# Kernel optimization log

Measured on AMD Instinct MI355X. Metric: run time of the kernel, lower is better.

Reference implementation:

```python
import jax, jax.numpy as jnp
import numpy as np

GRID_SIZE = 5
SPLINE_ORDER = 3
NUM_COEFF = GRID_SIZE + SPLINE_ORDER  # 8
L = 3
B, I, H = 4096, 256, 512
EPS = 1e-5


def make_grid(in_features):
    # efficient-kan default grid over [-1, 1] extended by spline_order knots each side
    h = 2.0 / GRID_SIZE
    g = jnp.arange(-SPLINE_ORDER, GRID_SIZE + SPLINE_ORDER + 1, dtype=jnp.float32) * h - 1.0
    return jnp.broadcast_to(g, (in_features, g.shape[0]))  # (in, G+2k+1)


def b_splines(x, grid):
    # x: (B, in), grid: (in, G+2k+1) -> (B, in, G+k) via Cox-de-Boor recursion
    xg = x[..., None]
    bases = ((xg >= grid[:, :-1]) & (xg < grid[:, 1:])).astype(x.dtype)
    for j in range(1, SPLINE_ORDER + 1):
        left = (xg - grid[:, :-(j + 1)]) / (grid[:, j:-1] - grid[:, :-(j + 1)])
        right = (grid[:, j + 1:] - xg) / (grid[:, j + 1:] - grid[:, 1:-j])
        bases = left * bases[..., :-1] + right * bases[..., 1:]
    return bases


def kan_linear(x, base_w, spline_w, grid):
    # base path: SiLU(x) @ W_base^T ; spline path: sum over (in, coeff)
    base = jax.nn.silu(x) @ base_w.T
    spl = jnp.einsum('bik,oik->bo', b_splines(x, grid), spline_w)
    return base + spl


def layer_norm(x, g, b):
    mu = jnp.mean(x, axis=-1, keepdims=True)
    var = jnp.var(x, axis=-1, keepdims=True)
    return (x - mu) / jnp.sqrt(var + EPS) * g + b


def _sublayer(z_prev, wx_b, wx_s, wh_b, wh_s, hz_b, hz_s, phi_b, phi_s,
              hh_w, hh_b, ln_g, ln_b, x_t, grid_in, grid_h):
    s_t = kan_linear(x_t, wx_b, wx_s, grid_in) + kan_linear(z_prev, wh_b, wh_s, grid_h)
    o_t = kan_linear(s_t, phi_b, phi_s, grid_h)
    z_t = layer_norm(z_prev @ hh_w.T + hh_b + kan_linear(o_t, hz_b, hz_s, grid_h), ln_g, ln_b)
    return o_t, z_t


def setup_inputs() -> dict:
    key = jax.random.key(0)
    ks = jax.random.split(key, 24)
    s = 0.05  # small init to keep gates/splines in sane range
    inp = {
        'x_t': jax.random.normal(ks[0], (B, I), jnp.float32),
        'h_prev': jax.random.normal(ks[1], (B, H), jnp.float32),
        'c_prev': jax.random.normal(ks[2], (B, H), jnp.float32),
        'z_prev': jax.random.normal(ks[3], (L, B, H), jnp.float32),
        'wx_base': jax.random.normal(ks[4], (L, H, I), jnp.float32) * s,
        'wx_spline': jax.random.normal(ks[5], (L, H, I, NUM_COEFF), jnp.float32) * s,
        'wh_base': jax.random.normal(ks[6], (L, H, H), jnp.float32) * s,
        'wh_spline': jax.random.normal(ks[7], (L, H, H, NUM_COEFF), jnp.float32) * s,
        'hz_base': jax.random.normal(ks[8], (L, H, H), jnp.float32) * s,
        'hz_spline': jax.random.normal(ks[9], (L, H, H, NUM_COEFF), jnp.float32) * s,
        'phi_base': jax.random.normal(ks[10], (L, H, H), jnp.float32) * s,
        'phi_spline': jax.random.normal(ks[11], (L, H, H, NUM_COEFF), jnp.float32) * s,
        'hh_w': jax.random.normal(ks[12], (L, H, H), jnp.float32) * s,
        'hh_b': jax.random.normal(ks[13], (L, H), jnp.float32) * s,
        'ln_g': jnp.ones((L, H), jnp.float32),
        'ln_b': jnp.zeros((L, H), jnp.float32),
        'f_w': jax.random.normal(ks[14], (H, I + H), jnp.float32) * s,
        'f_b': jax.random.normal(ks[15], (H,), jnp.float32) * s,
        'i_w': jax.random.normal(ks[16], (H, I + H), jnp.float32) * s,
        'i_b': jax.random.normal(ks[17], (H,), jnp.float32) * s,
        'g_w': jax.random.normal(ks[18], (H, I + H), jnp.float32) * s,
        'g_b': jax.random.normal(ks[19], (H,), jnp.float32) * s,
        'o_w': jax.random.normal(ks[20], (H, L * H), jnp.float32) * s,
        'o_b': jax.random.normal(ks[21], (H,), jnp.float32) * s,
    }
    return inp


def reference(x_t, h_prev, c_prev, z_prev, wx_base, wx_spline, wh_base, wh_spline,
              hz_base, hz_spline, phi_base, phi_spline, hh_w, hh_b, ln_g, ln_b,
              f_w, f_b, i_w, i_b, g_w, g_b, o_w, o_b):
    grid_in = make_grid(I)
    grid_h = make_grid(H)
    cat = jnp.concatenate([x_t, h_prev], axis=-1)  # (B, I+H)
    f_t = jax.nn.sigmoid(cat @ f_w.T + f_b)
    i_t = jax.nn.sigmoid(cat @ i_w.T + i_b)
    g_t = jnp.tanh(cat @ g_w.T + g_b)
    # vmap the RKAN sublayer over the L stacked sublayers
    sub = jax.vmap(_sublayer, in_axes=(0,) * 13 + (None, None, None))
    o_all, z_all = sub(z_prev, wx_base, wx_spline, wh_base, wh_spline,
                       hz_base, hz_spline, phi_base, phi_spline,
                       hh_w, hh_b, ln_g, ln_b, x_t, grid_in, grid_h)
    # concat sublayer phi outputs: (L,B,H) -> (B, L*H)
    r_t = jnp.transpose(o_all, (1, 0, 2)).reshape(B, L * H)
    o_t = jax.nn.sigmoid(r_t @ o_w.T + o_b)
    c_t = f_t * c_prev + i_t * g_t
    h_t = o_t * jnp.tanh(c_t)
    return h_t, c_t, z_all
```

## Files before the change

kernel.cpp:

```cpp
#include <hip/hip_runtime.h>

typedef __attribute__((ext_vector_type(8))) short short8;
typedef __attribute__((ext_vector_type(4))) float floatx4;

__device__ inline short f2bf(float v) {
    unsigned u = __builtin_bit_cast(unsigned, v);
    unsigned r = (u + 0x7fffu + ((u >> 16) & 1u)) >> 16;
    return (short)r;
}
__device__ inline float bf2f(short s) {
    unsigned u = ((unsigned)(unsigned short)s) << 16;
    return __builtin_bit_cast(float, u);
}

__device__ inline void spline8(float v, short* arr) {
    float u = (v + 2.2f) * 2.5f;
    float fj = floorf(u);
    int jj = (int)fj;
    float t1 = u - fj;
    float ok = (jj >= 0 && jj <= 10) ? (1.f / 6.f) : 0.f;
    float t2 = t1 * t1, t3 = t2 * t1;
    float omt = 1.f - t1;
    short sw0 = f2bf(omt * omt * omt * ok);
    short sw1 = f2bf((3.f * t3 - 6.f * t2 + 4.f) * ok);
    short sw2 = f2bf((-3.f * t3 + 3.f * t2 + 3.f * t1 + 1.f) * ok);
    short sw3 = f2bf(t3 * ok);
#pragma unroll
    for (int s = 0; s < 8; ++s) {
        int rr = s - jj + 3;
        arr[s] = (rr == 0) ? sw0 : (rr == 1) ? sw1 : (rr == 2) ? sw2
                 : (rr == 3) ? sw3 : (short)0;
    }
}

__global__ __launch_bounds__(256, 3) void gemm128(
    int S, int Kh,
    const short* __restrict__ A0, int lda0, long sA0, int K0,
    const short* __restrict__ W0, int ldw0, long sW0,
    const short* __restrict__ A1, int lda1, long sA1, int K1,
    const short* __restrict__ W1, int ldw1, long sW1,
    float* __restrict__ C, int ldc, long sC, long sSplit)
{
    __shared__ short As[128 * 32];
    __shared__ short Ws[128 * 32];
    const int t = threadIdx.x;
    int n = blockIdx.x + (blockIdx.y << 5) + (blockIdx.z << 7);
    int k8 = n & 7, j = n >> 3;
    int byi = j & 3;
    int t2 = j >> 2;
    int bxi = k8 * 4 + (t2 & 3);
    int bzi = t2 >> 2;
    const int z = bzi / S, s = bzi % S;
    const int bm = bxi * 128, bn = byi * 128;
    const int lane = t & 63, w = t >> 6;
    const int wm = (w >> 1) * 64, wn = (w & 1) * 64;
    const int lrow = lane & 15, quad = lane >> 4;

    floatx4 acc[4][4] = {};

    const int kbeg = s * Kh, kend = kbeg + Kh;

    const short* A = A0 + (long)z * sA0;
    const short* W = W0 + (long)z * sW0;
    int lda = lda0, ldw = ldw0;
    int kb = kbeg, ke = (kend < K0) ? kend : K0;

    for (int seg = 0; seg < 2; ++seg) {
        for (int kv = kb; kv < ke; kv += 32) {
#pragma unroll
            for (int cj = 0; cj < 2; ++cj) {
                int c = cj * 256 + t;
                int row = c >> 2, cg = (c & 3) * 8;
                const short* gp = A + (long)(bm + row) * lda + kv + cg;
                __builtin_amdgcn_global_load_lds(
                    (const __attribute__((address_space(1))) void*)gp,
                    (__attribute__((address_space(3))) void*)(As + c * 8), 16, 0, 0);
                const short* gq = W + (long)(bn + row) * ldw + kv + cg;
                __builtin_amdgcn_global_load_lds(
                    (const __attribute__((address_space(1))) void*)gq,
                    (__attribute__((address_space(3))) void*)(Ws + c * 8), 16, 0, 0);
            }
            __syncthreads();
            short8 af[4], bfr[4];
#pragma unroll
            for (int mi = 0; mi < 4; ++mi)
                af[mi] = *(const short8*)(As + (wm + mi * 16 + lrow) * 32 + quad * 8);
#pragma unroll
            for (int ni = 0; ni < 4; ++ni)
                bfr[ni] = *(const short8*)(Ws + (wn + ni * 16 + lrow) * 32 + quad * 8);
#pragma unroll
            for (int mi = 0; mi < 4; ++mi)
#pragma unroll
                for (int ni = 0; ni < 4; ++ni)
                    acc[mi][ni] = __builtin_amdgcn_mfma_f32_16x16x32_bf16(
                        af[mi], bfr[ni], acc[mi][ni], 0, 0, 0);
            __syncthreads();
        }
        A = A1 + (long)z * sA1;
        W = W1 + (long)z * sW1;
        lda = lda1; ldw = ldw1;
        kb = ((kbeg > K0) ? kbeg : K0) - K0;
        ke = kend - K0;
    }

    float* Cz = C + (long)z * sC + (long)s * sSplit;
#pragma unroll
    for (int mi = 0; mi < 4; ++mi)
#pragma unroll
        for (int ni = 0; ni < 4; ++ni)
#pragma unroll
            for (int r = 0; r < 4; ++r) {
                int row = bm + wm + mi * 16 + quad * 4 + r;
                int col = bn + wn + ni * 16 + lrow;
                Cz[(long)row * ldc + col] = acc[mi][ni][r];
            }
}

__global__ __launch_bounds__(256) void gemm64(
    int swz,
    const short* __restrict__ A0, int lda0, long sA0, int K0,
    const short* __restrict__ W0, int ldw0, long sW0,
    const short* __restrict__ A1, int lda1, long sA1, int K1,
    const short* __restrict__ W1, int ldw1, long sW1,
    short* __restrict__ C, int ldc, long sC)
{
    __shared__ short As[64 * 32];
    __shared__ short Ws[128 * 32];
    const int t = threadIdx.x;
    int bxi = blockIdx.x, byi = blockIdx.y, bzi = blockIdx.z;
    if (swz) {
        int n = bxi + (byi << 6) + (bzi << 8);
        int k = n & 7, j = n >> 3;
        byi = j & 3;
        bxi = k * 8 + ((j >> 2) & 7);
        bzi = j >> 5;
    }
    const int z = bzi;
    const int bm = bxi * 64;
    const int bn = byi * 128;
    const int lane = t & 63, w = t >> 6;
    const int wm = (w >> 1) * 32, wn = (w & 1) * 64;
    const int lrow = lane & 15, quad = lane >> 4;

    floatx4 acc[2][4] = {};

    const short* A = A0 + (long)z * sA0;
    const short* W = W0 + (long)z * sW0;
    int K = K0, lda = lda0, ldw = ldw0;

    for (int seg = 0; seg < 2; ++seg) {
        for (int k0 = 0; k0 < K; k0 += 32) {
            {
                int row = t >> 2, cg = (t & 3) * 8;
                const short* gp = A + (long)(bm + row) * lda + k0 + cg;
                __builtin_amdgcn_global_load_lds(
                    (const __attribute__((address_space(1))) void*)gp,
                    (__attribute__((address_space(3))) void*)(As + t * 8), 16, 0, 0);
            }
#pragma unroll
            for (int j = 0; j < 2; ++j) {
                int cj = j * 256 + t;
                int row = cj >> 2, cg = (cj & 3) * 8;
                const short* gq = W + (long)(bn + row) * ldw + k0 + cg;
                __builtin_amdgcn_global_load_lds(
                    (const __attribute__((address_space(1))) void*)gq,
                    (__attribute__((address_space(3))) void*)(Ws + cj * 8), 16, 0, 0);
            }
            __syncthreads();
            short8 af[2], bfr[4];
#pragma unroll
            for (int mi = 0; mi < 2; ++mi)
                af[mi] = *(const short8*)(As + (wm + mi * 16 + lrow) * 32 + quad * 8);
#pragma unroll
            for (int ni = 0; ni < 4; ++ni)
                bfr[ni] = *(const short8*)(Ws + (wn + ni * 16 + lrow) * 32 + quad * 8);
#pragma unroll
            for (int mi = 0; mi < 2; ++mi)
#pragma unroll
                for (int ni = 0; ni < 4; ++ni)
                    acc[mi][ni] = __builtin_amdgcn_mfma_f32_16x16x32_bf16(
                        af[mi], bfr[ni], acc[mi][ni], 0, 0, 0);
            __syncthreads();
        }
        A = A1 + (long)z * sA1; W = W1 + (long)z * sW1;
        K = K1; lda = lda1; ldw = ldw1;
    }

    short* Cz = C + (long)z * sC;
#pragma unroll
    for (int mi = 0; mi < 2; ++mi)
#pragma unroll
        for (int ni = 0; ni < 4; ++ni)
#pragma unroll
            for (int r = 0; r < 4; ++r) {
                int row = bm + wm + mi * 16 + quad * 4 + r;
                int col = bn + wn + ni * 16 + lrow;
                Cz[(long)row * ldc + col] = f2bf(acc[mi][ni][r]);
            }
}

__global__ __launch_bounds__(256) void megapack(
    const float* __restrict__ wx_b, const float* __restrict__ wx_s,
    const float* __restrict__ wh_b, const float* __restrict__ wh_s,
    const float* __restrict__ hz_b, const float* __restrict__ hz_s,
    const float* __restrict__ phi_b, const float* __restrict__ phi_s,
    const float* __restrict__ hh_w, const float* __restrict__ o_w,
    const float* __restrict__ f_w, const float* __restrict__ i_w,
    const float* __restrict__ g_w,
    short* __restrict__ Wx, short* __restrict__ Wh, short* __restrict__ Whz,
    short* __restrict__ Wphi, short* __restrict__ HHb, short* __restrict__ OWb,
    short* __restrict__ Wg)
{
    int bid = blockIdx.x, tid = threadIdx.x;
    if (bid < 13824) {
        long idx = (long)bid * 256 + tid;
        int r = (int)(idx / 2304), c = (int)(idx % 2304);
        float v = (c < 256) ? wx_b[(long)r * 256 + c]
                            : wx_s[(long)r * 2048 + (c - 256)];
        Wx[idx] = f2bf(v);
    } else if (bid < 96768) {
        int jb = bid - 13824;
        int job = jb / 27648, lb = jb % 27648;
        const float* bp = (job == 0) ? wh_b : (job == 1) ? hz_b : phi_b;
        const float* sp = (job == 0) ? wh_s : (job == 1) ? hz_s : phi_s;
        short* dp = (job == 0) ? Wh : (job == 1) ? Whz : Wphi;
        long idx = (long)lb * 256 + tid;
        int r = (int)(idx / 4608), c = (int)(idx % 4608);
        float v = (c < 512) ? bp[(long)r * 512 + c]
                            : sp[(long)r * 4096 + (c - 512)];
        dp[idx] = f2bf(v);
    } else if (bid < 99840) {
        long idx = (long)(bid - 96768) * 256 + tid;
        HHb[idx] = f2bf(hh_w[idx]);
    } else if (bid < 102912) {
        long idx = (long)(bid - 99840) * 256 + tid;
        OWb[idx] = f2bf(o_w[idx]);
    } else if (bid < 104448) {
        long idx = (long)(bid - 102912) * 256 + tid;
        Wg[idx] = f2bf(f_w[idx]);
    } else if (bid < 105984) {
        long idx = (long)(bid - 104448) * 256 + tid;
        Wg[393216 + idx] = f2bf(i_w[idx]);
    } else {
        long idx = (long)(bid - 105984) * 256 + tid;
        Wg[786432 + idx] = f2bf(g_w[idx]);
    }
}

__global__ __launch_bounds__(256) void prep_acts(
    const float* __restrict__ x_t, const float* __restrict__ h_prev,
    const float* __restrict__ z_prev,
    short* __restrict__ Xe, short* __restrict__ Agate,
    short* __restrict__ Ze, short* __restrict__ zraw)
{
    int bid = blockIdx.x, tid = threadIdx.x;
    if (bid < 4096) {
        int r = bid, i = tid;
        float v = x_t[(long)r * 256 + i];
        Agate[(long)r * 768 + i] = f2bf(v);
        long ob = (long)r * 2304;
        Xe[ob + i] = f2bf(v / (1.f + __expf(-v)));
        short arr[8];
        spline8(v, arr);
        *(short8*)(Xe + ob + 256 + (long)i * 8) = *(const short8*)arr;
    } else if (bid < 12288) {
        long idx = (long)(bid - 4096) * 256 + tid;
        long b = idx >> 9; int hh = (int)(idx & 511);
        Agate[b * 768 + 256 + hh] = f2bf(h_prev[idx]);
    } else {
        int j = bid - 12288;
        int r = j >> 1, i = (j & 1) * 256 + tid;
        float v = z_prev[(long)r * 512 + i];
        zraw[(long)r * 512 + i] = f2bf(v);
        long ob = (long)r * 4608;
        Ze[ob + i] = f2bf(v / (1.f + __expf(-v)));
        short arr[8];
        spline8(v, arr);
        *(short8*)(Ze + ob + 512 + (long)i * 8) = *(const short8*)arr;
    }
}

__global__ __launch_bounds__(256) void expand_pair(
    const float* __restrict__ P, long split_off, int inF,
    short* __restrict__ out, short* __restrict__ compact)
{
    int i = blockIdx.x * 256 + threadIdx.x;
    int r = blockIdx.y;
    long idx = (long)r * inF + i;
    float v = P[idx] + P[idx + split_off];
    if (compact) compact[idx] = f2bf(v);

    long ob = (long)r * inF * 9;
    out[ob + i] = f2bf(v / (1.f + __expf(-v)));

    short arr[8];
    spline8(v, arr);
    *(short8*)(out + ob + inF + (long)i * 8) = *(const short8*)arr;
}

__global__ __launch_bounds__(256) void ln_pair(const float* __restrict__ P,
                                               long split_off,
                                               const float* __restrict__ hh_b,
                                               const float* __restrict__ ln_g,
                                               const float* __restrict__ ln_b,
                                               float* __restrict__ out)
{
    int row = blockIdx.x;
    int l = row >> 12;
    int t = threadIdx.x;
    long base = (long)row * 512;
    float v0 = P[base + t]       + P[base + t + split_off]       + hh_b[l * 512 + t];
    float v1 = P[base + t + 256] + P[base + t + 256 + split_off] + hh_b[l * 512 + t + 256];
    float s = v0 + v1, sq = v0 * v0 + v1 * v1;
#pragma unroll
    for (int off = 32; off; off >>= 1) {
        s += __shfl_down(s, off);
        sq += __shfl_down(sq, off);
    }
    __shared__ float ls[4], lq[4];
    int w = t >> 6, lane = t & 63;
    if (lane == 0) { ls[w] = s; lq[w] = sq; }
    __syncthreads();
    float S = ls[0] + ls[1] + ls[2] + ls[3];
    float Q = lq[0] + lq[1] + lq[2] + lq[3];
    float mu = S * (1.f / 512.f);
    float var = Q * (1.f / 512.f) - mu * mu;
    float rstd = rsqrtf(var + 1e-5f);
    float* o = out + (long)row * 512;
    o[t]       = (v0 - mu) * rstd * ln_g[l * 512 + t]       + ln_b[l * 512 + t];
    o[t + 256] = (v1 - mu) * rstd * ln_g[l * 512 + t + 256] + ln_b[l * 512 + t + 256];
}

__global__ __launch_bounds__(256) void cell_epilogue(const short* __restrict__ gates,
                                                     const short* __restrict__ opre,
                                                     const float* __restrict__ c_prev,
                                                     const float* __restrict__ f_b,
                                                     const float* __restrict__ i_b,
                                                     const float* __restrict__ g_b,
                                                     const float* __restrict__ o_b,
                                                     float* __restrict__ out)
{
    long idx = blockIdx.x * 256L + threadIdx.x;
    long b = idx >> 9; int h = (int)(idx & 511);
    const short* g = gates + b * 1536;
    float fp = bf2f(g[h]) + f_b[h];
    float ip = bf2f(g[512 + h]) + i_b[h];
    float gp = bf2f(g[1024 + h]) + g_b[h];
    float op = bf2f(opre[idx]) + o_b[h];
    float ft = 1.f / (1.f + __expf(-fp));
    float it = 1.f / (1.f + __expf(-ip));
    float gt = tanhf(gp);
    float ot = 1.f / (1.f + __expf(-op));
    float c = ft * c_prev[idx] + it * gt;
    out[idx] = ot * tanhf(c);
    out[idx + 2097152] = c;
}

extern "C" void kernel_launch(void* const* d_in, const int* in_sizes, int n_in,
                              void* d_out, int out_size, void* d_ws, size_t ws_size,
                              hipStream_t stream)
{
    const float* x_t       = (const float*)d_in[0];
    const float* h_prev    = (const float*)d_in[1];
    const float* c_prev    = (const float*)d_in[2];
    const float* z_prev    = (const float*)d_in[3];
    const float* wx_base   = (const float*)d_in[4];
    const float* wx_spline = (const float*)d_in[5];
    const float* wh_base   = (const float*)d_in[6];
    const float* wh_spline = (const float*)d_in[7];
    const float* hz_base   = (const float*)d_in[8];
    const float* hz_spline = (const float*)d_in[9];
    const float* phi_base  = (const float*)d_in[10];
    const float* phi_spline= (const float*)d_in[11];
    const float* hh_w      = (const float*)d_in[12];
    const float* hh_b      = (const float*)d_in[13];
    const float* ln_g      = (const float*)d_in[14];
    const float* ln_b      = (const float*)d_in[15];
    const float* f_w       = (const float*)d_in[16];
    const float* f_b       = (const float*)d_in[17];
    const float* i_w       = (const float*)d_in[18];
    const float* i_b       = (const float*)d_in[19];
    const float* g_w       = (const float*)d_in[20];
    const float* g_b       = (const float*)d_in[21];
    const float* o_w       = (const float*)d_in[22];
    const float* o_b       = (const float*)d_in[23];
    float* out = (float*)d_out;
    const long BH = 4096L * 512;

    char* p = (char*)d_ws;
    auto alloc = [&](size_t bytes) {
        char* q = p;
        p += (bytes + 255) & ~(size_t)255;
        return q;
    };

    short* Wx   = (short*)alloc(3L * 512 * 2304 * 2);
    short* Wh   = (short*)alloc(3L * 512 * 4608 * 2);
    short* Whz  = (short*)alloc(3L * 512 * 4608 * 2);
    short* Wphi = (short*)alloc(3L * 512 * 4608 * 2);
    short* HHb  = (short*)alloc(3L * 512 * 512 * 2);
    short* OWb  = (short*)alloc(512L * 1536 * 2);
    short* Wg   = (short*)alloc(1536L * 768 * 2);
    short* Agate= (short*)alloc(4096L * 768 * 2);
    short* zraw = (short*)alloc(3L * 4096 * 512 * 2);
    short* XR   = (short*)alloc(4096L * 2304 * 2);
    short* Ebuf = (short*)alloc(3L * 4096 * 4608 * 2);
    float* Pbuf = (float*)alloc(2L * 3 * 4096 * 512 * 4);
    short* Xe = XR;
    short* Rbuf = XR;
    short* gbuf = Ebuf;
    short* opre = Ebuf + 4096L * 1536;
    const long PS = 3L * 4096 * 512;

    megapack<<<107520, 256, 0, stream>>>(
        wx_base, wx_spline, wh_base, wh_spline, hz_base, hz_spline,
        phi_base, phi_spline, hh_w, o_w, f_w, i_w, g_w,
        Wx, Wh, Whz, Wphi, HHb, OWb, Wg);

    prep_acts<<<36864, 256, 0, stream>>>(x_t, h_prev, z_prev, Xe, Agate, Ebuf, zraw);

    gemm128<<<dim3(32, 4, 6), 256, 0, stream>>>(2, 3456,
        Xe, 2304, 0, 2304,                 Wx, 2304, 512L * 2304,
        Ebuf, 4608, 4096L * 4608, 4608,    Wh, 4608, 512L * 4608,
        Pbuf, 512, 4096L * 512, PS);

    expand_pair<<<dim3(2, 12288), 256, 0, stream>>>(Pbuf, PS, 512, Ebuf, (short*)0);

    gemm128<<<dim3(32, 4, 6), 256, 0, stream>>>(2, 2304,
        Ebuf, 4608, 4096L * 4608, 4608,    Wphi, 4608, 512L * 4608,
        zraw, 0, 0, 0,                     Wphi, 0, 0,
        Pbuf, 1536, 512, PS);

    expand_pair<<<dim3(2, 12288), 256, 0, stream>>>(Pbuf, PS, 512, Ebuf, Rbuf);

    gemm128<<<dim3(32, 4, 6), 256, 0, stream>>>(2, 2560,
        Ebuf, 13824, 4608, 4608,           Whz, 4608, 512L * 4608,
        zraw, 512, 4096L * 512, 512,       HHb, 512, 512L * 512,
        Pbuf, 512, 4096L * 512, PS);

    ln_pair<<<12288, 256, 0, stream>>>(Pbuf, PS, hh_b, ln_g, ln_b, out + 2 * BH);

    gemm64<<<dim3(64, 12, 1), 256, 0, stream>>>(0,
        Agate, 768, 0, 768,  Wg, 768, 0,
        Agate, 768, 0, 0,    Wg, 768, 0,
        gbuf, 1536, 0);

    gemm64<<<dim3(64, 4, 1), 256, 0, stream>>>(0,
        Rbuf, 1536, 0, 1536, OWb, 1536, 0,
        Rbuf, 1536, 0, 0,    OWb, 1536, 0,
        opre, 512, 0);

    cell_epilogue<<<8192, 256, 0, stream>>>(gbuf, opre, c_prev, f_b, i_b, g_b, o_b, out);
}
```

Baseline: 740.8 us.

## Enlarge GEMM tiles to 256x128 with 512 threads and raise split-K to four

The main bf16 GEMM kernel now computes 256x128 output tiles with 8 waves per block instead of 128x128 with 4 waves, so each W tile loaded into LDS is reused across more rows. When the workspace is large enough, split-K goes from 2 to 4 to keep enough blocks in flight despite the larger tiles. The expand and layernorm kernels sum a variable number of partial buffers, and expand handles two elements per thread. The weight-packing kernel converts four floats per thread with float4 loads. Split-K of 4 doubles the fp32 partial-sum traffic and the reduction work, and the larger tile raises LDS and register use per block.

```diff
diff --git a/kernel.cpp b/kernel.cpp
--- a/kernel.cpp
+++ b/kernel.cpp
@@ -33,7 +33,7 @@
     }
 }
 
-__global__ __launch_bounds__(256, 3) void gemm128(
+__global__ __launch_bounds__(512, 4) void gemm256(
     int S, int Kh,
     const short* __restrict__ A0, int lda0, long sA0, int K0,
     const short* __restrict__ W0, int ldw0, long sW0,
@@ -41,17 +41,16 @@
     const short* __restrict__ W1, int ldw1, long sW1,
     float* __restrict__ C, int ldc, long sC, long sSplit)
 {
-    __shared__ short As[128 * 32];
+    __shared__ short As[256 * 32];
     __shared__ short Ws[128 * 32];
     const int t = threadIdx.x;
-    int n = blockIdx.x + (blockIdx.y << 5) + (blockIdx.z << 7);
+    int n = blockIdx.x + (blockIdx.y << 4) + (blockIdx.z << 6);
     int k8 = n & 7, j = n >> 3;
     int byi = j & 3;
-    int t2 = j >> 2;
-    int bxi = k8 * 4 + (t2 & 3);
-    int bzi = t2 >> 2;
+    int bxi = (k8 << 1) + ((j >> 2) & 1);
+    int bzi = j >> 3;
     const int z = bzi / S, s = bzi % S;
-    const int bm = bxi * 128, bn = byi * 128;
+    const int bm = bxi * 256, bn = byi * 128;
     const int lane = t & 63, w = t >> 6;
     const int wm = (w >> 1) * 64, wn = (w & 1) * 64;
     const int lrow = lane & 15, quad = lane >> 4;
@@ -68,17 +67,20 @@
     for (int seg = 0; seg < 2; ++seg) {
         for (int kv = kb; kv < ke; kv += 32) {
 #pragma unroll
-            for (int cj = 0; cj < 2; ++cj) {
-                int c = cj * 256 + t;
+            for (int i = 0; i < 2; ++i) {
+                int c = i * 512 + t;
                 int row = c >> 2, cg = (c & 3) * 8;
                 const short* gp = A + (long)(bm + row) * lda + kv + cg;
                 __builtin_amdgcn_global_load_lds(
                     (const __attribute__((address_space(1))) void*)gp,
                     (__attribute__((address_space(3))) void*)(As + c * 8), 16, 0, 0);
+            }
+            {
+                int row = t >> 2, cg = (t & 3) * 8;
                 const short* gq = W + (long)(bn + row) * ldw + kv + cg;
                 __builtin_amdgcn_global_load_lds(
                     (const __attribute__((address_space(1))) void*)gq,
-                    (__attribute__((address_space(3))) void*)(Ws + c * 8), 16, 0, 0);
+                    (__attribute__((address_space(3))) void*)(Ws + t * 8), 16, 0, 0);
             }
             __syncthreads();
             short8 af[4], bfr[4];
@@ -199,7 +201,7 @@
             }
 }
 
-__global__ __launch_bounds__(256) void megapack(
+__global__ __launch_bounds__(256) void megapack4(
     const float* __restrict__ wx_b, const float* __restrict__ wx_s,
     const float* __restrict__ wh_b, const float* __restrict__ wh_s,
     const float* __restrict__ hz_b, const float* __restrict__ hz_s,
@@ -212,39 +214,49 @@
     short* __restrict__ Wg)
 {
     int bid = blockIdx.x, tid = threadIdx.x;
-    if (bid < 13824) {
-        long idx = (long)bid * 256 + tid;
-        int r = (int)(idx / 2304), c = (int)(idx % 2304);
-        float v = (c < 256) ? wx_b[(long)r * 256 + c]
-                            : wx_s[(long)r * 2048 + (c - 256)];
-        Wx[idx] = f2bf(v);
-    } else if (bid < 96768) {
-        int jb = bid - 13824;
-        int job = jb / 27648, lb = jb % 27648;
+    float4 v;
+    short* dst;
+    long e;
+    if (bid < 3456) {
+        e = ((long)bid * 256 + tid) * 4;
+        int r = (int)(e / 2304), c = (int)(e % 2304);
+        v = (c < 256) ? *(const float4*)(wx_b + (long)r * 256 + c)
+                      : *(const float4*)(wx_s + (long)r * 2048 + (c - 256));
+        dst = Wx + e;
+    } else if (bid < 24192) {
+        int jb = bid - 3456;
+        int job = jb / 6912, lb = jb % 6912;
         const float* bp = (job == 0) ? wh_b : (job == 1) ? hz_b : phi_b;
         const float* sp = (job == 0) ? wh_s : (job == 1) ? hz_s : phi_s;
         short* dp = (job == 0) ? Wh : (job == 1) ? Whz : Wphi;
-        long idx = (long)lb * 256 + tid;
-        int r = (int)(idx / 4608), c = (int)(idx % 4608);
-        float v = (c < 512) ? bp[(long)r * 512 + c]
-                            : sp[(long)r * 4096 + (c - 512)];
-        dp[idx] = f2bf(v);
-    } else if (bid < 99840) {
-        long idx = (long)(bid - 96768) * 256 + tid;
-        HHb[idx] = f2bf(hh_w[idx]);
-    } else if (bid < 102912) {
-        long idx = (long)(bid - 99840) * 256 + tid;
-        OWb[idx] = f2bf(o_w[idx]);
-    } else if (bid < 104448) {
-        long idx = (long)(bid - 102912) * 256 + tid;
-        Wg[idx] = f2bf(f_w[idx]);
-    } else if (bid < 105984) {
-        long idx = (long)(bid - 104448) * 256 + tid;
-        Wg[393216 + idx] = f2bf(i_w[idx]);
+        e = ((long)lb * 256 + tid) * 4;
+        int r = (int)(e / 4608), c = (int)(e % 4608);
+        v = (c < 512) ? *(const float4*)(bp + (long)r * 512 + c)
+                      : *(const float4*)(sp + (long)r * 4096 + (c - 512));
+        dst = dp + e;
+    } else if (bid < 24960) {
+        e = ((long)(bid - 24192) * 256 + tid) * 4;
+        v = *(const float4*)(hh_w + e);
+        dst = HHb + e;
+    } else if (bid < 25728) {
+        e = ((long)(bid - 24960) * 256 + tid) * 4;
+        v = *(const float4*)(o_w + e);
+        dst = OWb + e;
+    } else if (bid < 26112) {
+        e = ((long)(bid - 25728) * 256 + tid) * 4;
+        v = *(const float4*)(f_w + e);
+        dst = Wg + e;
+    } else if (bid < 26496) {
+        e = ((long)(bid - 26112) * 256 + tid) * 4;
+        v = *(const float4*)(i_w + e);
+        dst = Wg + 393216 + e;
     } else {
-        long idx = (long)(bid - 105984) * 256 + tid;
-        Wg[786432 + idx] = f2bf(g_w[idx]);
-    }
+        e = ((long)(bid - 26496) * 256 + tid) * 4;
+        v = *(const float4*)(g_w + e);
+        dst = Wg + 786432 + e;
+    }
+    dst[0] = f2bf(v.x); dst[1] = f2bf(v.y);
+    dst[2] = f2bf(v.z); dst[3] = f2bf(v.w);
 }
 
 __global__ __launch_bounds__(256) void prep_acts(
@@ -281,25 +293,32 @@
 }
 
 __global__ __launch_bounds__(256) void expand_pair(
-    const float* __restrict__ P, long split_off, int inF,
+    const float* __restrict__ P, long sSplit, int S, int inF,
     short* __restrict__ out, short* __restrict__ compact)
 {
-    int i = blockIdx.x * 256 + threadIdx.x;
+    int i = (blockIdx.x * 256 + threadIdx.x) * 2;
     int r = blockIdx.y;
     long idx = (long)r * inF + i;
-    float v = P[idx] + P[idx + split_off];
-    if (compact) compact[idx] = f2bf(v);
+    float2 v = *(const float2*)(P + idx);
+    for (int s = 1; s < S; ++s) {
+        float2 a = *(const float2*)(P + idx + (long)s * sSplit);
+        v.x += a.x; v.y += a.y;
+    }
+    if (compact) { compact[idx] = f2bf(v.x); compact[idx + 1] = f2bf(v.y); }
 
     long ob = (long)r * inF * 9;
-    out[ob + i] = f2bf(v / (1.f + __expf(-v)));
+    out[ob + i]     = f2bf(v.x / (1.f + __expf(-v.x)));
+    out[ob + i + 1] = f2bf(v.y / (1.f + __expf(-v.y)));
 
     short arr[8];
-    spline8(v, arr);
+    spline8(v.x, arr);
     *(short8*)(out + ob + inF + (long)i * 8) = *(const short8*)arr;
+    spline8(v.y, arr);
+    *(short8*)(out + ob + inF + (long)(i + 1) * 8) = *(const short8*)arr;
 }
 
 __global__ __launch_bounds__(256) void ln_pair(const float* __restrict__ P,
-                                               long split_off,
+                                               long sSplit, int S,
                                                const float* __restrict__ hh_b,
                                                const float* __restrict__ ln_g,
                                                const float* __restrict__ ln_b,
@@ -309,21 +328,25 @@
     int l = row >> 12;
     int t = threadIdx.x;
     long base = (long)row * 512;
-    float v0 = P[base + t]       + P[base + t + split_off]       + hh_b[l * 512 + t];
-    float v1 = P[base + t + 256] + P[base + t + 256 + split_off] + hh_b[l * 512 + t + 256];
-    float s = v0 + v1, sq = v0 * v0 + v1 * v1;
+    float v0 = hh_b[l * 512 + t];
+    float v1 = hh_b[l * 512 + t + 256];
+    for (int s = 0; s < S; ++s) {
+        v0 += P[base + t + (long)s * sSplit];
+        v1 += P[base + t + 256 + (long)s * sSplit];
+    }
+    float sm = v0 + v1, sq = v0 * v0 + v1 * v1;
 #pragma unroll
     for (int off = 32; off; off >>= 1) {
-        s += __shfl_down(s, off);
+        sm += __shfl_down(sm, off);
         sq += __shfl_down(sq, off);
     }
     __shared__ float ls[4], lq[4];
     int w = t >> 6, lane = t & 63;
-    if (lane == 0) { ls[w] = s; lq[w] = sq; }
+    if (lane == 0) { ls[w] = sm; lq[w] = sq; }
     __syncthreads();
-    float S = ls[0] + ls[1] + ls[2] + ls[3];
+    float Sm = ls[0] + ls[1] + ls[2] + ls[3];
     float Q = lq[0] + lq[1] + lq[2] + lq[3];
-    float mu = S * (1.f / 512.f);
+    float mu = Sm * (1.f / 512.f);
     float var = Q * (1.f / 512.f) - mu * mu;
     float rstd = rsqrtf(var + 1e-5f);
     float* o = out + (long)row * 512;
@@ -405,40 +428,45 @@
     short* zraw = (short*)alloc(3L * 4096 * 512 * 2);
     short* XR   = (short*)alloc(4096L * 2304 * 2);
     short* Ebuf = (short*)alloc(3L * 4096 * 4608 * 2);
-    float* Pbuf = (float*)alloc(2L * 3 * 4096 * 512 * 4);
+
+    const long PS = 3L * 4096 * 512;
+    size_t used = (size_t)(p - (char*)d_ws);
+    size_t splitB = (size_t)PS * 4;
+    int S = (ws_size >= used + 4 * splitB + 4096) ? 4 : 2;
+    float* Pbuf = (float*)alloc((size_t)S * splitB);
+
     short* Xe = XR;
     short* Rbuf = XR;
     short* gbuf = Ebuf;
     short* opre = Ebuf + 4096L * 1536;
-    const long PS = 3L * 4096 * 512;
-
-    megapack<<<107520, 256, 0, stream>>>(
+
+    megapack4<<<26880, 256, 0, stream>>>(
         wx_base, wx_spline, wh_base, wh_spline, hz_base, hz_spline,
         phi_base, phi_spline, hh_w, o_w, f_w, i_w, g_w,
         Wx, Wh, Whz, Wphi, HHb, OWb, Wg);
 
     prep_acts<<<36864, 256, 0, stream>>>(x_t, h_prev, z_prev, Xe, Agate, Ebuf, zraw);
 
-    gemm128<<<dim3(32, 4, 6), 256, 0, stream>>>(2, 3456,
+    gemm256<<<dim3(16, 4, 3 * S), 512, 0, stream>>>(S, 6912 / S,
         Xe, 2304, 0, 2304,                 Wx, 2304, 512L * 2304,
         Ebuf, 4608, 4096L * 4608, 4608,    Wh, 4608, 512L * 4608,
         Pbuf, 512, 4096L * 512, PS);
 
-    expand_pair<<<dim3(2, 12288), 256, 0, stream>>>(Pbuf, PS, 512, Ebuf, (short*)0);
-
-    gemm128<<<dim3(32, 4, 6), 256, 0, stream>>>(2, 2304,
+    expand_pair<<<dim3(1, 12288), 256, 0, stream>>>(Pbuf, PS, S, 512, Ebuf, (short*)0);
+
+    gemm256<<<dim3(16, 4, 3 * S), 512, 0, stream>>>(S, 4608 / S,
         Ebuf, 4608, 4096L * 4608, 4608,    Wphi, 4608, 512L * 4608,
         zraw, 0, 0, 0,                     Wphi, 0, 0,
         Pbuf, 1536, 512, PS);
 
-    expand_pair<<<dim3(2, 12288), 256, 0, stream>>>(Pbuf, PS, 512, Ebuf, Rbuf);
-
-    gemm128<<<dim3(32, 4, 6), 256, 0, stream>>>(2, 2560,
+    expand_pair<<<dim3(1, 12288), 256, 0, stream>>>(Pbuf, PS, S, 512, Ebuf, Rbuf);
+
+    gemm256<<<dim3(16, 4, 3 * S), 512, 0, stream>>>(S, 5120 / S,
         Ebuf, 13824, 4608, 4608,           Whz, 4608, 512L * 4608,
         zraw, 512, 4096L * 512, 512,       HHb, 512, 512L * 512,
         Pbuf, 512, 4096L * 512, PS);
 
-    ln_pair<<<12288, 256, 0, stream>>>(Pbuf, PS, hh_b, ln_g, ln_b, out + 2 * BH);
+    ln_pair<<<12288, 256, 0, stream>>>(Pbuf, PS, S, hh_b, ln_g, ln_b, out + 2 * BH);
 
     gemm64<<<dim3(64, 12, 1), 256, 0, stream>>>(0,
         Agate, 768, 0, 768,  Wg, 768, 0,
```

After: 770.2 us. 1.04x slower.
